# Kernel tuning notes

Measured on AMD Instinct MI355X. Metric: run time of the kernel, lower is better.

## Reference

```python
import jax, jax.numpy as jnp
import numpy as np

B, T, D, H = 2, 2048, 2048, 16
HD = D // H  # 128
HALF = HD // 2  # 64


def _apply_rotary(x, cos, sin):
    """x: (B,H,T,HD); cos/sin: (T, HD//2). Interleaved rotation matching torch ref."""
    half = x.shape[-1] // 2
    x1, x2 = x[..., :half], x[..., half:]
    c = cos[None, None, :, :]
    s = sin[None, None, :, :]
    # stack on last axis then flatten -> out[...,2i]=x1*c-x2*s, out[...,2i+1]=x1*s+x2*c
    return jnp.stack([x1 * c - x2 * s, x1 * s + x2 * c], axis=-1).reshape(x.shape)


def setup_inputs() -> dict:
    key = jax.random.key(0)
    k1, k2, k3 = jax.random.split(key, 3)
    x = jax.random.normal(k1, (B, T, D), dtype=jnp.float32)
    # realistic RoPE tables: theta = 10000^{-2i/HD}
    inv_freq = 1.0 / (10000.0 ** (np.arange(0, HALF, dtype=np.float32) * 2.0 / HD))
    ang = np.arange(T, dtype=np.float32)[:, None] * inv_freq[None, :]  # (T, HALF)
    cos = jnp.asarray(np.cos(ang), dtype=jnp.float32)
    sin = jnp.asarray(np.sin(ang), dtype=jnp.float32)
    Wqkv = jax.random.normal(k2, (D, 3 * D), dtype=jnp.float32) * (D ** -0.5)
    Wproj = jax.random.normal(k3, (D, D), dtype=jnp.float32) * (D ** -0.5)
    return {"x": x, "cos": cos, "sin": sin, "Wqkv": Wqkv, "Wproj": Wproj}


def reference(x, cos, sin, Wqkv, Wproj):
    b, t, d = x.shape
    qkv = (x @ Wqkv).reshape(b, t, 3, H, HD)
    q = jnp.transpose(qkv[:, :, 0], (0, 2, 1, 3))  # (B,H,T,HD)
    k = jnp.transpose(qkv[:, :, 1], (0, 2, 1, 3))
    v = jnp.transpose(qkv[:, :, 2], (0, 2, 1, 3))
    q = _apply_rotary(q, cos, sin)
    k = _apply_rotary(k, cos, sin)
    scale = 1.0 / jnp.sqrt(jnp.asarray(HD, dtype=x.dtype))
    scores = jnp.einsum("bhqd,bhkd->bhqk", q, k) * scale
    causal = jnp.tril(jnp.ones((t, t), dtype=bool))
    scores = jnp.where(causal[None, None], scores, jnp.finfo(x.dtype).min)
    attn = jax.nn.softmax(scores, axis=-1)
    out = jnp.einsum("bhqk,bhkd->bhqd", attn, v)
    out = jnp.transpose(out, (0, 2, 1, 3)).reshape(b, t, d)
    return out @ Wproj
```

## Files before the change

kernel.cpp:

```cpp
#include <hip/hip_runtime.h>
#include <hip/hip_bf16.h>

#define B_  2
#define T_  2048
#define D_  2048
#define H_  16
#define HD_ 128
#define NT_ 4096
#define D3_ 6144

typedef __bf16 bf16;
typedef _Float16 f16;
typedef bf16 bf16x2 __attribute__((ext_vector_type(2)));
typedef bf16 bf16x4 __attribute__((ext_vector_type(4)));
typedef bf16 bf16x8 __attribute__((ext_vector_type(8)));
typedef f16  f16x2  __attribute__((ext_vector_type(2)));
typedef f16  f16x4  __attribute__((ext_vector_type(4)));
typedef float floatx4 __attribute__((ext_vector_type(4)));

__device__ __forceinline__ void gl_lds16(const void* g, void* l) {
    __builtin_amdgcn_global_load_lds((const __attribute__((address_space(1))) void*)g,
                                     (__attribute__((address_space(3))) void*)l, 16, 0, 0);
}

__global__ __launch_bounds__(256) void k_prep(const float* __restrict__ x,
                                              const float* __restrict__ Wqkv, const float* __restrict__ Wproj,
                                              bf16* __restrict__ xb, bf16* __restrict__ WqkvT, bf16* __restrict__ WprojT) {
    int blk = blockIdx.x;
    int tid = threadIdx.x;
    if (blk < 8192) {
        int i = blk * 256 + tid;
        float4 v = ((const float4*)x)[i];
        bf16x4 o = { (bf16)v.x, (bf16)v.y, (bf16)v.z, (bf16)v.w };
        ((bf16x4*)xb)[i] = o;
        return;
    }
    __shared__ float tile[64][65];
    const float* in; bf16* out; int C, bx;
    if (blk < 8192 + 3072) { bx = blk - 8192; in = Wqkv; out = WqkvT; C = D3_; }
    else                   { bx = blk - 8192 - 3072; in = Wproj; out = WprojT; C = D_; }
    const int R = D_;
    int nbx = C / 64;
    int c0 = (bx % nbx) * 64, r0 = (bx / nbx) * 64;
#pragma unroll
    for (int i = 0; i < 16; i++) {
        int idx = tid + i * 256, r = idx >> 6, c = idx & 63;
        tile[r][c] = in[(size_t)(r0 + r) * C + (c0 + c)];
    }
    __syncthreads();
#pragma unroll
    for (int i = 0; i < 16; i++) {
        int idx = tid + i * 256, r = idx >> 6, c = idx & 63;
        out[(size_t)(c0 + r) * R + (r0 + c)] = (bf16)tile[c][r];
    }
}

__global__ __launch_bounds__(512, 1) void k_gemm_qkv(const bf16* __restrict__ A, const bf16* __restrict__ Bt,
                                                     const float* __restrict__ cosp, const float* __restrict__ sinp,
                                                     bf16* __restrict__ Qg, bf16* __restrict__ Kg, f16* __restrict__ VTg) {
    __shared__ bf16 smem[3 * 24576];
    const int tid = threadIdx.x, wid = tid >> 6, lane = tid & 63;
    const int quad = lane >> 4, l16 = lane & 15;
    const int n0 = blockIdx.x * 128, m0 = blockIdx.y * 256;
    const int wr = (wid >> 1) * 64, wc = (wid & 1) * 64;
    const bf16* Ablk = A + (size_t)m0 * D_;
    const bf16* Bblk = Bt + (size_t)n0 * D_;
    const int sgch = (lane & 7) ^ (lane >> 3);
    const int aHalf = (wid >> 2) * 8192;
    const int rAbase = ((wid >> 1) & 1) * 64;
    const int coA = (rAbase + l16) * 64;
    const int coB = 16384 + (wc + l16) * 64;
    floatx4 acc[4][4] = {};

#define QKV_STAGE(KT, BUFO, JJ) do {                                                    \
        int cI_ = (JJ) * 512 + wid * 64 + lane;                                         \
        const bf16* gsrc_;                                                              \
        if ((JJ) < 4) gsrc_ = Ablk + (size_t)(cI_ >> 3) * D_ + (KT) * 64 + sgch * 8;    \
        else          gsrc_ = Bblk + (size_t)((cI_ >> 3) - 256) * D_ + (KT) * 64 + sgch * 8; \
        gl_lds16(gsrc_, smem + (BUFO) + ((JJ) * 512 + wid * 64) * 8);                   \
    } while (0)

#pragma unroll
    for (int j = 0; j < 6; j++) QKV_STAGE(0, 0, j);
#pragma unroll
    for (int j = 0; j < 6; j++) QKV_STAGE(1, 24576, j);
    asm volatile("s_waitcnt vmcnt(6)" ::: "memory");
    __builtin_amdgcn_s_barrier();

    int bcur = 0, bpre = 2;
    for (int t = 0; t < 32; t++) {
        const int bb = bcur * 24576;
        const int po = bpre * 24576;
        const int kpre = t + 2;
        const bool dopre = (kpre < 32);
        bf16x8 af[4][2], bfr[4][2];
#pragma unroll
        for (int mt = 0; mt < 4; mt++)
#pragma unroll
            for (int kc = 0; kc < 2; kc++)
                af[mt][kc] = *(const bf16x8*)(smem + bb + aHalf + coA + mt * 1024 + (((kc * 4 + quad) ^ (l16 & 7)) * 8));
#pragma unroll
        for (int nt = 0; nt < 4; nt++)
#pragma unroll
            for (int kc = 0; kc < 2; kc++)
                bfr[nt][kc] = *(const bf16x8*)(smem + bb + coB + nt * 1024 + (((kc * 4 + quad) ^ (l16 & 7)) * 8));
        if (dopre) {
            QKV_STAGE(kpre, po, 0); QKV_STAGE(kpre, po, 1); QKV_STAGE(kpre, po, 2);
            QKV_STAGE(kpre, po, 3); QKV_STAGE(kpre, po, 4); QKV_STAGE(kpre, po, 5);
        }
        __builtin_amdgcn_s_setprio(1);
#pragma unroll
        for (int mt = 0; mt < 4; mt++)
#pragma unroll
            for (int nt = 0; nt < 4; nt++)
#pragma unroll
                for (int kc = 0; kc < 2; kc++)
                    acc[mt][nt] = __builtin_amdgcn_mfma_f32_16x16x32_bf16(af[mt][kc], bfr[nt][kc], acc[mt][nt], 0, 0, 0);
        __builtin_amdgcn_s_setprio(0);
        if (t == 30) asm volatile("s_waitcnt vmcnt(0)" ::: "memory");
        else         asm volatile("s_waitcnt vmcnt(6)" ::: "memory");
        __builtin_amdgcn_s_barrier();
        bcur = (bcur == 2) ? 0 : bcur + 1;
        bpre = (bpre == 2) ? 0 : bpre + 1;
    }
#undef QKV_STAGE

    bf16* const stage = smem;
#pragma unroll
    for (int mt = 0; mt < 4; mt++)
#pragma unroll
        for (int nt = 0; nt < 4; nt++)
#pragma unroll
            for (int r = 0; r < 4; r++)
                stage[(wr + mt * 16 + quad * 4 + r) * 130 + wc + nt * 16 + l16] = (bf16)acc[mt][nt][r];
    __syncthreads();
    const int type = n0 >> 11, h = (n0 & 2047) >> 7;
    const int b = m0 >> 11, t0 = m0 & 2047;
    if (type < 2) {
        bf16* out = (type == 0 ? Qg : Kg) + ((size_t)(b * H_ + h) * T_ + t0) * HD_;
#pragma unroll
        for (int it = 0; it < 32; it++) {
            int idx = it * 512 + tid, tl = idx >> 6, i = idx & 63;
            float c = cosp[(t0 + tl) * 64 + i], s = sinp[(t0 + tl) * 64 + i];
            float x1 = (float)stage[tl * 130 + i], x2 = (float)stage[tl * 130 + 64 + i];
            bf16x2 o = { (bf16)(x1 * c - x2 * s), (bf16)(x1 * s + x2 * c) };
            *(bf16x2*)(out + (size_t)tl * HD_ + 2 * i) = o;
        }
    } else {
        f16* out = VTg + (size_t)(b * H_ + h) * HD_ * T_ + t0;
#pragma unroll
        for (int it = 0; it < 32; it++) {
            int idx = it * 512 + tid, d = idx >> 7, tp = (idx & 127) * 2;
            f16x2 o = { (f16)(float)stage[tp * 130 + d], (f16)(float)stage[(tp + 1) * 130 + d] };
            *(f16x2*)(out + (size_t)d * T_ + tp) = o;
        }
    }
}

__global__ __launch_bounds__(512, 1) void k_proj(const bf16* __restrict__ A, const bf16* __restrict__ Bt,
                                                 float* __restrict__ C) {
    __shared__ bf16 smem[3 * 24576];
    const int tid = threadIdx.x, wid = tid >> 6, lane = tid & 63;
    const int quad = lane >> 4, l16 = lane & 15;
    const int n0 = blockIdx.x * 128, m0 = blockIdx.y * 256;
    const int wr = (wid >> 1) * 64, wc = (wid & 1) * 64;
    const bf16* Ablk = A + (size_t)m0 * D_;
    const bf16* Bblk = Bt + (size_t)n0 * D_;
    const int sgch = (lane & 7) ^ (lane >> 3);
    const int aHalf = (wid >> 2) * 8192;
    const int rAbase = ((wid >> 1) & 1) * 64;
    const int coA = (rAbase + l16) * 64;
    const int coB = 16384 + (wc + l16) * 64;
    floatx4 acc[4][4] = {};

#define PRJ_STAGE(KT, BUFO, JJ) do {                                                    \
        int cI_ = (JJ) * 512 + wid * 64 + lane;                                         \
        const bf16* gsrc_;                                                              \
        if ((JJ) < 4) gsrc_ = Ablk + (size_t)(cI_ >> 3) * D_ + (KT) * 64 + sgch * 8;    \
        else          gsrc_ = Bblk + (size_t)((cI_ >> 3) - 256) * D_ + (KT) * 64 + sgch * 8; \
        gl_lds16(gsrc_, smem + (BUFO) + ((JJ) * 512 + wid * 64) * 8);                   \
    } while (0)

#pragma unroll
    for (int j = 0; j < 6; j++) PRJ_STAGE(0, 0, j);
#pragma unroll
    for (int j = 0; j < 6; j++) PRJ_STAGE(1, 24576, j);
    asm volatile("s_waitcnt vmcnt(6)" ::: "memory");
    __builtin_amdgcn_s_barrier();

    int bcur = 0, bpre = 2;
    for (int t = 0; t < 32; t++) {
        const int bb = bcur * 24576;
        const int po = bpre * 24576;
        const int kpre = t + 2;
        const bool dopre = (kpre < 32);
        bf16x8 af[4][2], bfr[4][2];
#pragma unroll
        for (int mt = 0; mt < 4; mt++)
#pragma unroll
            for (int kc = 0; kc < 2; kc++)
                af[mt][kc] = *(const bf16x8*)(smem + bb + aHalf + coA + mt * 1024 + (((kc * 4 + quad) ^ (l16 & 7)) * 8));
#pragma unroll
        for (int nt = 0; nt < 4; nt++)
#pragma unroll
            for (int kc = 0; kc < 2; kc++)
                bfr[nt][kc] = *(const bf16x8*)(smem + bb + coB + nt * 1024 + (((kc * 4 + quad) ^ (l16 & 7)) * 8));
        if (dopre) {
            PRJ_STAGE(kpre, po, 0); PRJ_STAGE(kpre, po, 1); PRJ_STAGE(kpre, po, 2);
            PRJ_STAGE(kpre, po, 3); PRJ_STAGE(kpre, po, 4); PRJ_STAGE(kpre, po, 5);
        }
        __builtin_amdgcn_s_setprio(1);
#pragma unroll
        for (int mt = 0; mt < 4; mt++)
#pragma unroll
            for (int nt = 0; nt < 4; nt++)
#pragma unroll
                for (int kc = 0; kc < 2; kc++)
                    acc[mt][nt] = __builtin_amdgcn_mfma_f32_16x16x32_bf16(af[mt][kc], bfr[nt][kc], acc[mt][nt], 0, 0, 0);
        __builtin_amdgcn_s_setprio(0);
        if (t == 30) asm volatile("s_waitcnt vmcnt(0)" ::: "memory");
        else         asm volatile("s_waitcnt vmcnt(6)" ::: "memory");
        __builtin_amdgcn_s_barrier();
        bcur = (bcur == 2) ? 0 : bcur + 1;
        bpre = (bpre == 2) ? 0 : bpre + 1;
    }
#undef PRJ_STAGE

#pragma unroll
    for (int mt = 0; mt < 4; mt++)
#pragma unroll
        for (int nt = 0; nt < 4; nt++)
#pragma unroll
            for (int r = 0; r < 4; r++) {
                int row = m0 + wr + mt * 16 + quad * 4 + r;
                int col = n0 + wc + nt * 16 + l16;
                C[(size_t)row * D_ + col] = acc[mt][nt][r];
            }
}

__global__ __launch_bounds__(256, 2) void k_flash(const bf16* __restrict__ Qg, const bf16* __restrict__ Kg,
                                                  const f16* __restrict__ VTg, bf16* __restrict__ Og) {
    __shared__ bf16 Ksh[64 * 128];
    __shared__ f16  Vsh[128 * 64];
    const int b1 = blockIdx.x;
    const int bh = b1 & 31;
    const int qt = (b1 < 256) ? (15 - (b1 >> 5)) : ((b1 - 256) >> 5);
    const int tid = threadIdx.x, w = tid >> 6, lane = tid & 63;
    const int quad = lane >> 4, l16 = lane & 15;
    const float scale2 = 0.08838834764831845f * 1.4426950408889634f;
    const int wrow = w * 32;
    const bf16* Qb = Qg + ((size_t)bh * T_ + qt * 128) * HD_;
    bf16x8 qf[2][4];
#pragma unroll
    for (int mt = 0; mt < 2; mt++)
#pragma unroll
        for (int kc = 0; kc < 4; kc++)
            qf[mt][kc] = *(const bf16x8*)(Qb + (size_t)(wrow + mt * 16 + l16) * HD_ + kc * 32 + quad * 8);
    floatx4 oaccT[8][2] = {};
    float lsum[2] = { 0.f, 0.f };
    const int nkt = 2 * (qt + 1);
    for (int kt = 0; kt < nkt; kt++) {
        __syncthreads();
        const bf16* Kt = Kg + ((size_t)bh * T_ + kt * 64) * HD_;
        const f16*  Vt = VTg + (size_t)bh * HD_ * T_ + kt * 64;
#pragma unroll
        for (int i = 0; i < 4; i++) {
            int ch = w * 4 + i;
            {
                int row = ch * 4 + (lane >> 4);
                int c = (lane & 15) ^ (row & 7);
                gl_lds16(Kt + (size_t)row * HD_ + c * 8, Ksh + ch * 512);
            }
            {
                int row = ch * 8 + (lane >> 3);
                int c = (lane & 7) ^ (row & 7);
                gl_lds16(Vt + (size_t)row * T_ + c * 8, Vsh + ch * 512);
            }
        }
        __syncthreads();
        const bool diag = (kt >= 2 * qt);
        f16x4 pf[2][4];
#pragma unroll
        for (int nt = 0; nt < 4; nt++) {
            floatx4 s0 = {}, s1 = {};
#pragma unroll
            for (int kc = 0; kc < 4; kc++) {
                bf16x8 kf = *(const bf16x8*)(Ksh + (nt * 16 + l16) * 128 + (((kc * 4 + quad) ^ (l16 & 7)) * 8));
                s0 = __builtin_amdgcn_mfma_f32_16x16x32_bf16(kf, qf[0][kc], s0, 0, 0, 0);
                s1 = __builtin_amdgcn_mfma_f32_16x16x32_bf16(kf, qf[1][kc], s1, 0, 0, 0);
            }
#pragma unroll
            for (int r = 0; r < 4; r++) {
                float v0 = s0[r] * scale2, v1 = s1[r] * scale2;
                if (diag) {
                    int gk = kt * 64 + nt * 16 + quad * 4 + r;
                    if (gk > qt * 128 + wrow + l16) v0 = -1e30f;
                    if (gk > qt * 128 + wrow + 16 + l16) v1 = -1e30f;
                }
                float p0 = exp2f(v0), p1 = exp2f(v1);
                lsum[0] += p0; lsum[1] += p1;
                pf[0][nt][r] = (f16)p0; pf[1][nt][r] = (f16)p1;
            }
        }
#pragma unroll
        for (int nt = 0; nt < 4; nt++)
#pragma unroll
            for (int dt = 0; dt < 8; dt++) {
                int row = dt * 16 + l16;
                f16x4 vf = *(const f16x4*)(Vsh + row * 64 + (((nt * 2 + (quad >> 1)) ^ (row & 7)) * 8) + (quad & 1) * 4);
#pragma unroll
                for (int mt = 0; mt < 2; mt++)
                    oaccT[dt][mt] = __builtin_amdgcn_mfma_f32_16x16x16f16(vf, pf[mt][nt], oaccT[dt][mt], 0, 0, 0);
            }
    }
    const int b = bh >> 4, h = bh & 15;
    float inv[2];
#pragma unroll
    for (int mt = 0; mt < 2; mt++) {
        float l = lsum[mt];
        l += __shfl_xor(l, 16);
        l += __shfl_xor(l, 32);
        inv[mt] = 1.0f / l;
    }
#pragma unroll
    for (int mt = 0; mt < 2; mt++) {
        int t = qt * 128 + wrow + mt * 16 + l16;
#pragma unroll
        for (int dt = 0; dt < 8; dt++) {
            bf16x4 o;
#pragma unroll
            for (int r = 0; r < 4; r++) o[r] = (bf16)(oaccT[dt][mt][r] * inv[mt]);
            int c = h * HD_ + dt * 16 + quad * 4;
            *(bf16x4*)(Og + (size_t)(b * T_ + t) * D_ + c) = o;
        }
    }
}

extern "C" void kernel_launch(void* const* d_in, const int* in_sizes, int n_in,
                              void* d_out, int out_size, void* d_ws, size_t ws_size,
                              hipStream_t stream) {
    const float* x     = (const float*)d_in[0];
    const float* cosp  = (const float*)d_in[1];
    const float* sinp  = (const float*)d_in[2];
    const float* Wqkv  = (const float*)d_in[3];
    const float* Wproj = (const float*)d_in[4];
    float* out = (float*)d_out;
    char* ws = (char*)d_ws;
    bf16* xb     = (bf16*)(ws);
    bf16* WqkvT  = (bf16*)(ws + (size_t)(16u << 20));
    bf16* WprojT = (bf16*)(ws + (size_t)(40u << 20));
    bf16* Qg     = (bf16*)(ws + (size_t)(48u << 20));
    bf16* Kg     = (bf16*)(ws + (size_t)(64u << 20));
    f16*  VTg    = (f16*) (ws + (size_t)(80u << 20));
    bf16* Og     = xb;

    k_prep<<<dim3(8192 + 3072 + 1024), 256, 0, stream>>>(x, Wqkv, Wproj, xb, WqkvT, WprojT);
    k_gemm_qkv<<<dim3(D3_ / 128, NT_ / 256), 512, 0, stream>>>(xb, WqkvT, cosp, sinp, Qg, Kg, VTg);
    k_flash<<<dim3(512), 256, 0, stream>>>(Qg, Kg, VTg, Og);
    k_proj<<<dim3(D_ / 128, NT_ / 256), 512, 0, stream>>>(Og, WprojT, out);
}
```

Before: 357.2 us.

## Double-buffer LDS fragment reads across MFMA halves in GEMM main loops

Both GEMM main loops (QKV and projection) now use a shared, manually software-pipelined loop. Each k-step's MFMA work is split into two halves, and the LDS fragment reads for the next k-step are issued right after the barrier, between those halves. Two register sets of A/B fragments alternate, and the loop is unrolled by two with rotating buffer offsets. The aim is to hide LDS read latency behind matrix-core work. The cost is roughly double the fragment register use and a more rigid instruction schedule.

```diff
diff --git a/kernel.cpp b/kernel.cpp
--- a/kernel.cpp
+++ b/kernel.cpp
@@ -54,6 +54,62 @@
         out[(size_t)(c0 + r) * R + (r0 + c)] = (bf16)tile[c][r];
     }
 }
+
+
+#define G_STAGE(KT, BUFO, JJ) do {                                                      \
+        int cI_ = (JJ) * 512 + wid * 64 + lane;                                         \
+        const bf16* gsrc_;                                                              \
+        if ((JJ) < 4) gsrc_ = Ablk + (size_t)(cI_ >> 3) * D_ + (KT) * 64 + sgch * 8;    \
+        else          gsrc_ = Bblk + (size_t)((cI_ >> 3) - 256) * D_ + (KT) * 64 + sgch * 8; \
+        gl_lds16(gsrc_, smem + (BUFO) + ((JJ) * 512 + wid * 64) * 8);                   \
+    } while (0)
+
+#define G_READ(BUFO, AF, BF) do {                                                       \
+        _Pragma("unroll") for (int mt_ = 0; mt_ < 4; mt_++)                             \
+        _Pragma("unroll") for (int kc_ = 0; kc_ < 2; kc_++)                             \
+            AF[mt_][kc_] = *(const bf16x8*)(smem + (BUFO) + aHalf + coA + mt_ * 1024 + (((kc_ * 4 + quad) ^ (l16 & 7)) * 8)); \
+        _Pragma("unroll") for (int nt_ = 0; nt_ < 4; nt_++)                             \
+        _Pragma("unroll") for (int kc_ = 0; kc_ < 2; kc_++)                             \
+            BF[nt_][kc_] = *(const bf16x8*)(smem + (BUFO) + coB + nt_ * 1024 + (((kc_ * 4 + quad) ^ (l16 & 7)) * 8)); \
+    } while (0)
+
+#define G_ITER(T, NXTO, PREO, CAF, CBF, NAF, NBF) do {                                  \
+        if ((T) + 2 < 32) {                                                             \
+            G_STAGE((T) + 2, (PREO), 0); G_STAGE((T) + 2, (PREO), 1);                   \
+            G_STAGE((T) + 2, (PREO), 2); G_STAGE((T) + 2, (PREO), 3);                   \
+            G_STAGE((T) + 2, (PREO), 4); G_STAGE((T) + 2, (PREO), 5);                   \
+        }                                                                               \
+        __builtin_amdgcn_s_setprio(1);                                                  \
+        _Pragma("unroll") for (int mt_ = 0; mt_ < 4; mt_++)                             \
+        _Pragma("unroll") for (int nt_ = 0; nt_ < 2; nt_++)                             \
+        _Pragma("unroll") for (int kc_ = 0; kc_ < 2; kc_++)                             \
+            acc[mt_][nt_] = __builtin_amdgcn_mfma_f32_16x16x32_bf16(CAF[mt_][kc_], CBF[nt_][kc_], acc[mt_][nt_], 0, 0, 0); \
+        __builtin_amdgcn_s_setprio(0);                                                  \
+        if ((T) >= 30) asm volatile("s_waitcnt vmcnt(0)" ::: "memory");                 \
+        else           asm volatile("s_waitcnt vmcnt(6)" ::: "memory");                 \
+        __builtin_amdgcn_s_barrier();                                                   \
+        if ((T) + 1 < 32) { G_READ((NXTO), NAF, NBF); }                                 \
+        __builtin_amdgcn_s_setprio(1);                                                  \
+        _Pragma("unroll") for (int mt_ = 0; mt_ < 4; mt_++)                             \
+        _Pragma("unroll") for (int nt_ = 2; nt_ < 4; nt_++)                             \
+        _Pragma("unroll") for (int kc_ = 0; kc_ < 2; kc_++)                             \
+            acc[mt_][nt_] = __builtin_amdgcn_mfma_f32_16x16x32_bf16(CAF[mt_][kc_], CBF[nt_][kc_], acc[mt_][nt_], 0, 0, 0); \
+        __builtin_amdgcn_s_setprio(0);                                                  \
+    } while (0)
+
+#define G_MAINLOOP()                                                                    \
+    _Pragma("unroll") for (int j = 0; j < 6; j++) G_STAGE(0, 0, j);                     \
+    _Pragma("unroll") for (int j = 0; j < 6; j++) G_STAGE(1, 24576, j);                 \
+    asm volatile("s_waitcnt vmcnt(6)" ::: "memory");                                    \
+    __builtin_amdgcn_s_barrier();                                                       \
+    bf16x8 afA[4][2], bfA[4][2], afB[4][2], bfB[4][2];                                  \
+    G_READ(0, afA, bfA);                                                                \
+    int b0 = 0, b1 = 24576, b2 = 49152;                                                 \
+    for (int t = 0; t < 32; t += 2) {                                                   \
+        G_ITER(t,     b1, b2, afA, bfA, afB, bfB);                                      \
+        G_ITER(t + 1, b2, b0, afB, bfB, afA, bfA);                                      \
+        int tmp_ = b0; b0 = b2; b2 = b1; b1 = tmp_;                                     \
+    }
 
 __global__ __launch_bounds__(512, 1) void k_gemm_qkv(const bf16* __restrict__ A, const bf16* __restrict__ Bt,
                                                      const float* __restrict__ cosp, const float* __restrict__ sinp,
@@ -72,58 +128,7 @@
     const int coB = 16384 + (wc + l16) * 64;
     floatx4 acc[4][4] = {};
 
-#define QKV_STAGE(KT, BUFO, JJ) do {                                                    \
-        int cI_ = (JJ) * 512 + wid * 64 + lane;                                         \
-        const bf16* gsrc_;                                                              \
-        if ((JJ) < 4) gsrc_ = Ablk + (size_t)(cI_ >> 3) * D_ + (KT) * 64 + sgch * 8;    \
-        else          gsrc_ = Bblk + (size_t)((cI_ >> 3) - 256) * D_ + (KT) * 64 + sgch * 8; \
-        gl_lds16(gsrc_, smem + (BUFO) + ((JJ) * 512 + wid * 64) * 8);                   \
-    } while (0)
-
-#pragma unroll
-    for (int j = 0; j < 6; j++) QKV_STAGE(0, 0, j);
-#pragma unroll
-    for (int j = 0; j < 6; j++) QKV_STAGE(1, 24576, j);
-    asm volatile("s_waitcnt vmcnt(6)" ::: "memory");
-    __builtin_amdgcn_s_barrier();
-
-    int bcur = 0, bpre = 2;
-    for (int t = 0; t < 32; t++) {
-        const int bb = bcur * 24576;
-        const int po = bpre * 24576;
-        const int kpre = t + 2;
-        const bool dopre = (kpre < 32);
-        bf16x8 af[4][2], bfr[4][2];
-#pragma unroll
-        for (int mt = 0; mt < 4; mt++)
-#pragma unroll
-            for (int kc = 0; kc < 2; kc++)
-                af[mt][kc] = *(const bf16x8*)(smem + bb + aHalf + coA + mt * 1024 + (((kc * 4 + quad) ^ (l16 & 7)) * 8));
-#pragma unroll
-        for (int nt = 0; nt < 4; nt++)
-#pragma unroll
-            for (int kc = 0; kc < 2; kc++)
-                bfr[nt][kc] = *(const bf16x8*)(smem + bb + coB + nt * 1024 + (((kc * 4 + quad) ^ (l16 & 7)) * 8));
-        if (dopre) {
-            QKV_STAGE(kpre, po, 0); QKV_STAGE(kpre, po, 1); QKV_STAGE(kpre, po, 2);
-            QKV_STAGE(kpre, po, 3); QKV_STAGE(kpre, po, 4); QKV_STAGE(kpre, po, 5);
-        }
-        __builtin_amdgcn_s_setprio(1);
-#pragma unroll
-        for (int mt = 0; mt < 4; mt++)
-#pragma unroll
-            for (int nt = 0; nt < 4; nt++)
-#pragma unroll
-                for (int kc = 0; kc < 2; kc++)
-                    acc[mt][nt] = __builtin_amdgcn_mfma_f32_16x16x32_bf16(af[mt][kc], bfr[nt][kc], acc[mt][nt], 0, 0, 0);
-        __builtin_amdgcn_s_setprio(0);
-        if (t == 30) asm volatile("s_waitcnt vmcnt(0)" ::: "memory");
-        else         asm volatile("s_waitcnt vmcnt(6)" ::: "memory");
-        __builtin_amdgcn_s_barrier();
-        bcur = (bcur == 2) ? 0 : bcur + 1;
-        bpre = (bpre == 2) ? 0 : bpre + 1;
-    }
-#undef QKV_STAGE
+    G_MAINLOOP()
 
     bf16* const stage = smem;
 #pragma unroll
@@ -173,58 +178,7 @@
     const int coB = 16384 + (wc + l16) * 64;
     floatx4 acc[4][4] = {};
 
-#define PRJ_STAGE(KT, BUFO, JJ) do {                                                    \
-        int cI_ = (JJ) * 512 + wid * 64 + lane;                                         \
-        const bf16* gsrc_;                                                              \
-        if ((JJ) < 4) gsrc_ = Ablk + (size_t)(cI_ >> 3) * D_ + (KT) * 64 + sgch * 8;    \
-        else          gsrc_ = Bblk + (size_t)((cI_ >> 3) - 256) * D_ + (KT) * 64 + sgch * 8; \
-        gl_lds16(gsrc_, smem + (BUFO) + ((JJ) * 512 + wid * 64) * 8);                   \
-    } while (0)
-
-#pragma unroll
-    for (int j = 0; j < 6; j++) PRJ_STAGE(0, 0, j);
-#pragma unroll
-    for (int j = 0; j < 6; j++) PRJ_STAGE(1, 24576, j);
-    asm volatile("s_waitcnt vmcnt(6)" ::: "memory");
-    __builtin_amdgcn_s_barrier();
-
-    int bcur = 0, bpre = 2;
-    for (int t = 0; t < 32; t++) {
-        const int bb = bcur * 24576;
-        const int po = bpre * 24576;
-        const int kpre = t + 2;
-        const bool dopre = (kpre < 32);
-        bf16x8 af[4][2], bfr[4][2];
-#pragma unroll
-        for (int mt = 0; mt < 4; mt++)
-#pragma unroll
-            for (int kc = 0; kc < 2; kc++)
-                af[mt][kc] = *(const bf16x8*)(smem + bb + aHalf + coA + mt * 1024 + (((kc * 4 + quad) ^ (l16 & 7)) * 8));
-#pragma unroll
-        for (int nt = 0; nt < 4; nt++)
-#pragma unroll
-            for (int kc = 0; kc < 2; kc++)
-                bfr[nt][kc] = *(const bf16x8*)(smem + bb + coB + nt * 1024 + (((kc * 4 + quad) ^ (l16 & 7)) * 8));
-        if (dopre) {
-            PRJ_STAGE(kpre, po, 0); PRJ_STAGE(kpre, po, 1); PRJ_STAGE(kpre, po, 2);
-            PRJ_STAGE(kpre, po, 3); PRJ_STAGE(kpre, po, 4); PRJ_STAGE(kpre, po, 5);
-        }
-        __builtin_amdgcn_s_setprio(1);
-#pragma unroll
-        for (int mt = 0; mt < 4; mt++)
-#pragma unroll
-            for (int nt = 0; nt < 4; nt++)
-#pragma unroll
-                for (int kc = 0; kc < 2; kc++)
-                    acc[mt][nt] = __builtin_amdgcn_mfma_f32_16x16x32_bf16(af[mt][kc], bfr[nt][kc], acc[mt][nt], 0, 0, 0);
-        __builtin_amdgcn_s_setprio(0);
-        if (t == 30) asm volatile("s_waitcnt vmcnt(0)" ::: "memory");
-        else         asm volatile("s_waitcnt vmcnt(6)" ::: "memory");
-        __builtin_amdgcn_s_barrier();
-        bcur = (bcur == 2) ? 0 : bcur + 1;
-        bpre = (bpre == 2) ? 0 : bpre + 1;
-    }
-#undef PRJ_STAGE
+    G_MAINLOOP()
 
 #pragma unroll
     for (int mt = 0; mt < 4; mt++)
```

After: 355.9 us. No clear change (-0.4%).
